# Optimization experiments

Measured on AMD Instinct MI355X. Metric: run time of the kernel, lower is better.

Reference implementation:

```python
import jax, jax.numpy as jnp
import numpy as np
from functools import partial

# Straight-through-estimator binarization: forward hard threshold,
# backward identity (matches BinaPs BinarizeTensorThresh autograd.Function).
@partial(jax.custom_vjp, nondiff_argnums=(1,))
def binarize(x, thresh):
    return (x >= thresh).astype(x.dtype)

def _bin_fwd(x, thresh):
    return binarize(x, thresh), None

def _bin_bwd(thresh, res, g):
    return (g,)

binarize.defvjp(_bin_fwd, _bin_bwd)

WEIGHT_THRESH = 0.5   # weightBClipValue passed to BinarizedLinearModule
ACT_THRESH = 1.0      # binary activation fires when pre-activation reaches 1


def setup_inputs() -> dict:
    key = jax.random.key(0)
    kx, kw = jax.random.split(key)
    B, D, H = 8192, 4096, 2048  # batch (transactions), features, hidden (patterns)
    x = (jax.random.uniform(kx, (B, D)) < 0.05).astype(jnp.float32)
    # Real-valued shared encoder weight, clipped to [-1, 1] by clipWeights();
    # init in [0, 1) so its 0.5-threshold binarization is non-trivial.
    W = jax.random.uniform(kw, (H, D), dtype=jnp.float32)
    b_enc = -jnp.ones((H,), jnp.float32)   # init_bias: vector of -1
    b0 = jnp.zeros((H,), jnp.float32)      # act0 bias (clipBias keeps <= 0)
    b3 = jnp.zeros((D,), jnp.float32)      # act3 bias (noBias forces 0)
    return {"x": x, "W": W, "b_enc": b_enc, "b0": b0, "b3": b3}


def reference(x, W, b_enc, b0, b3):
    # Binarize shared weight (encoder and transposed decoder use the same Wb)
    Wb = binarize(W, WEIGHT_THRESH)                      # [H, D] in {0,1}
    # Encoder: BinarizedLinear(D->H) with bias, then BinaryActivation
    h = binarize(x @ Wb.T + b_enc + b0, ACT_THRESH)      # [B, H] in {0,1}
    # Decoder: transposed shared weight, no bias, then final BinaryActivation
    out = binarize(h @ Wb + b3, ACT_THRESH)              # [B, D] in {0,1}
    return out
```

## Files before the change

kernel.cpp:

```cpp
#include <hip/hip_runtime.h>
#include <stdint.h>

#define BB 8192
#define DD 4096
#define HH 2048
#define DW (DD / 32)
#define HW (HH / 32)

__global__ void k_pack_x(const float* __restrict__ x,
                         uint32_t* __restrict__ xb) {
    int flat = blockIdx.x * blockDim.x + threadIdx.x;
    int b  = flat >> 7;
    int wd = flat & (DW - 1);
    const float4* p = (const float4*)(x + (size_t)b * DD + 32 * wd);
    uint32_t w = 0;
#pragma unroll
    for (int q = 0; q < 8; ++q) {
        float4 v = p[q];
        w |= (v.x >= 0.5f ? 1u : 0u) << (4 * q + 0);
        w |= (v.y >= 0.5f ? 1u : 0u) << (4 * q + 1);
        w |= (v.z >= 0.5f ? 1u : 0u) << (4 * q + 2);
        w |= (v.w >= 0.5f ? 1u : 0u) << (4 * q + 3);
    }
    xb[flat] = w;
}

__global__ void k_pack_wrow(const float* __restrict__ W,
                            uint32_t* __restrict__ WrowT4) {
    int flat = blockIdx.x * blockDim.x + threadIdx.x;
    int j = flat >> 7;
    int k = flat & (DW - 1);
    const float4* p = (const float4*)(W + (size_t)j * DD + 32 * k);
    uint32_t w = 0;
#pragma unroll
    for (int q = 0; q < 8; ++q) {
        float4 v = p[q];
        w |= (v.x >= 0.5f ? 1u : 0u) << (4 * q + 0);
        w |= (v.y >= 0.5f ? 1u : 0u) << (4 * q + 1);
        w |= (v.z >= 0.5f ? 1u : 0u) << (4 * q + 2);
        w |= (v.w >= 0.5f ? 1u : 0u) << (4 * q + 3);
    }
    WrowT4[((size_t)(k >> 2) * HH + j) * 4 + (k & 3)] = w;
}

__global__ void k_pack_wcol(const float* __restrict__ W,
                            uint32_t* __restrict__ WcolT) {
    int flat = blockIdx.x * blockDim.x + threadIdx.x;
    int kw = flat >> 12;
    int d  = flat & (DD - 1);
    uint32_t w = 0;
#pragma unroll
    for (int i = 0; i < 32; ++i) {
        float v = W[(size_t)(kw * 32 + i) * DD + d];
        w |= (v >= 0.5f ? 1u : 0u) << i;
    }
    WcolT[(size_t)kw * DD + d] = w;
}

__device__ __forceinline__ int calc_thresh(float bias) {
    float need = 1.0f - bias;
    if (!(need == need)) return 2000000000;
    if (need > 1.0e9f)  return 2000000000;
    if (need < -1.0e9f) return -2000000000;
    int t = (int)ceilf(need);
#pragma unroll
    for (int it = 0; it < 2; ++it)
        if ((float)(t - 1) + bias >= 1.0f) t--;
#pragma unroll
    for (int it = 0; it < 2; ++it)
        if ((float)t + bias < 1.0f) t++;
    return t;
}

__global__ void k_thresh(const float* __restrict__ b_enc,
                         const float* __restrict__ b0,
                         const float* __restrict__ b3,
                         int* __restrict__ t1, int* __restrict__ t2) {
    int tid = blockIdx.x * blockDim.x + threadIdx.x;
    if (tid < HH) {
        t1[tid] = calc_thresh(b_enc[tid] + b0[tid]);
    } else {
        int d = tid - HH;
        t2[d] = calc_thresh(b3[d]);
    }
}

__global__ void k_gemm1(const uint32_t* __restrict__ xb,
                        const uint4* __restrict__ WrowT4,
                        const int* __restrict__ t1,
                        uint32_t* __restrict__ hb) {
    int flat = blockIdx.x * blockDim.x + threadIdx.x;
    int b = flat >> 11;
    int j = flat & (HH - 1);
    const uint32_t* xr = xb + (size_t)b * DW;
    int t = t1[j];
    int c = 0;
    if (t > 0) {
        for (int k8 = 0; k8 < DW / 8; ++k8) {
            uint4 w0 = WrowT4[(size_t)(2 * k8) * HH + j];
            uint4 w1 = WrowT4[(size_t)(2 * k8 + 1) * HH + j];
            uint4 a0 = *(const uint4*)(xr + 8 * k8);
            uint4 a1 = *(const uint4*)(xr + 8 * k8 + 4);
            c += __popc(a0.x & w0.x) + __popc(a0.y & w0.y) +
                 __popc(a0.z & w0.z) + __popc(a0.w & w0.w) +
                 __popc(a1.x & w1.x) + __popc(a1.y & w1.y) +
                 __popc(a1.z & w1.z) + __popc(a1.w & w1.w);
            if (c >= t) break;
        }
    }
    unsigned long long m = __ballot(c >= t);
    if ((threadIdx.x & 63) == 0) {
        int jw = j >> 5;
        hb[(size_t)b * HW + jw]     = (uint32_t)m;
        hb[(size_t)b * HW + jw + 1] = (uint32_t)(m >> 32);
    }
}

__global__ void k_gemm2(const uint32_t* __restrict__ hb,
                        const uint32_t* __restrict__ WcolT,
                        const int* __restrict__ t2,
                        float* __restrict__ out) {
    int flat = blockIdx.x * blockDim.x + threadIdx.x;
    int b  = flat >> 10;
    int d0 = (flat & 1023) * 4;
    const uint32_t* hr = hb + (size_t)b * HW;
    int4 tt = *(const int4*)(t2 + d0);
    int c0 = 0, c1 = 0, c2 = 0, c3 = 0;
    for (int kw = 0; kw < HW; ++kw) {
        uint32_t h = hr[kw];
        uint4 w = *(const uint4*)(WcolT + (size_t)kw * DD + d0);
        c0 += __popc(h & w.x);
        c1 += __popc(h & w.y);
        c2 += __popc(h & w.z);
        c3 += __popc(h & w.w);
        if (c0 >= tt.x && c1 >= tt.y && c2 >= tt.z && c3 >= tt.w) break;
    }
    float4 r;
    r.x = (c0 >= tt.x) ? 1.0f : 0.0f;
    r.y = (c1 >= tt.y) ? 1.0f : 0.0f;
    r.z = (c2 >= tt.z) ? 1.0f : 0.0f;
    r.w = (c3 >= tt.w) ? 1.0f : 0.0f;
    *(float4*)(out + (size_t)b * DD + d0) = r;
}

extern "C" void kernel_launch(void* const* d_in, const int* in_sizes, int n_in,
                              void* d_out, int out_size, void* d_ws, size_t ws_size,
                              hipStream_t stream) {
    const float* x     = (const float*)d_in[0];
    const float* W     = (const float*)d_in[1];
    const float* b_enc = (const float*)d_in[2];
    const float* b0    = (const float*)d_in[3];
    const float* b3    = (const float*)d_in[4];
    float* out = (float*)d_out;

    char* ws = (char*)d_ws;
    uint32_t* WrowT4 = (uint32_t*)(ws);
    uint32_t* WcolT  = (uint32_t*)(ws + (1u << 20));
    uint32_t* xb     = (uint32_t*)(ws + (2u << 20));
    uint32_t* hb     = (uint32_t*)(ws + (6u << 20));
    int*      t1     = (int*)(ws + (8u << 20));
    int*      t2     = (int*)(ws + (8u << 20) + 8192);

    const int BLK = 256;

    k_pack_wrow<<<(HH * DW) / BLK, BLK, 0, stream>>>(W, WrowT4);
    k_pack_wcol<<<(HW * DD) / BLK, BLK, 0, stream>>>(W, WcolT);
    k_pack_x  <<<(BB * DW) / BLK, BLK, 0, stream>>>(x, xb);
    k_thresh  <<<(HH + DD) / BLK, BLK, 0, stream>>>(b_enc, b0, b3, t1, t2);
    k_gemm1   <<<(BB * HH) / BLK, BLK, 0, stream>>>(xb, (const uint4*)WrowT4, t1, hb);
    k_gemm2   <<<(BB * DD / 4) / BLK, BLK, 0, stream>>>(hb, WcolT, t2, out);
}
```

Before: 325.0 us.

## Fuse weight packing via LDS transpose and compute four batch rows per gemm1 thread

The two weight-packing kernels become one tiled kernel. It reads W once with coalesced float4 loads and builds the column-packed copy by transposing bits through shared memory, replacing the strided column reads. gemm1 now has each thread handle four batch rows for the same hidden unit, so every loaded packed-weight word is reused four times. The cost is an early exit that only fires when all four rows pass the threshold, plus higher register pressure from four accumulators.

Measured after the change: 304.5 us. 6.3% less time.

```diff
diff --git a/kernel.cpp b/kernel.cpp
--- a/kernel.cpp
+++ b/kernel.cpp
@@ -25,12 +25,20 @@
     xb[flat] = w;
 }
 
-__global__ void k_pack_wrow(const float* __restrict__ W,
-                            uint32_t* __restrict__ WrowT4) {
-    int flat = blockIdx.x * blockDim.x + threadIdx.x;
-    int j = flat >> 7;
-    int k = flat & (DW - 1);
-    const float4* p = (const float4*)(W + (size_t)j * DD + 32 * k);
+__global__ void __launch_bounds__(256)
+k_pack_w(const float* __restrict__ W,
+         uint32_t* __restrict__ WrowT4,
+         uint32_t* __restrict__ WcolT) {
+    __shared__ uint32_t lds[32][8];
+    int tile = blockIdx.x;
+    int jt = tile >> 4;
+    int dt = tile & 15;
+    int j0 = jt * 32;
+    int d0 = dt * 256;
+
+    int r  = threadIdx.x >> 3;
+    int wi = threadIdx.x & 7;
+    const float4* p = (const float4*)(W + (size_t)(j0 + r) * DD + d0 + wi * 32);
     uint32_t w = 0;
 #pragma unroll
     for (int q = 0; q < 8; ++q) {
@@ -40,21 +48,20 @@
         w |= (v.z >= 0.5f ? 1u : 0u) << (4 * q + 2);
         w |= (v.w >= 0.5f ? 1u : 0u) << (4 * q + 3);
     }
-    WrowT4[((size_t)(k >> 2) * HH + j) * 4 + (k & 3)] = w;
-}
-
-__global__ void k_pack_wcol(const float* __restrict__ W,
-                            uint32_t* __restrict__ WcolT) {
-    int flat = blockIdx.x * blockDim.x + threadIdx.x;
-    int kw = flat >> 12;
-    int d  = flat & (DD - 1);
-    uint32_t w = 0;
+    int k = dt * 8 + wi;
+    WrowT4[((size_t)(k >> 2) * HH + (j0 + r)) * 4 + (k & 3)] = w;
+    lds[r][wi] = w;
+    __syncthreads();
+
+    int dl = threadIdx.x;
+    int wsel = dl >> 5;
+    int bsel = dl & 31;
+    uint32_t cw = 0;
 #pragma unroll
     for (int i = 0; i < 32; ++i) {
-        float v = W[(size_t)(kw * 32 + i) * DD + d];
-        w |= (v >= 0.5f ? 1u : 0u) << i;
-    }
-    WcolT[(size_t)kw * DD + d] = w;
+        cw |= ((lds[i][wsel] >> bsel) & 1u) << i;
+    }
+    WcolT[(size_t)jt * DD + d0 + dl] = cw;
 }
 
 __device__ __forceinline__ int calc_thresh(float bias) {
@@ -90,29 +97,64 @@
                         const int* __restrict__ t1,
                         uint32_t* __restrict__ hb) {
     int flat = blockIdx.x * blockDim.x + threadIdx.x;
-    int b = flat >> 11;
-    int j = flat & (HH - 1);
-    const uint32_t* xr = xb + (size_t)b * DW;
+    int bg = flat >> 11;
+    int j  = flat & (HH - 1);
+    int b0 = bg * 4;
+    const uint32_t* xr0 = xb + (size_t)(b0 + 0) * DW;
+    const uint32_t* xr1 = xb + (size_t)(b0 + 1) * DW;
+    const uint32_t* xr2 = xb + (size_t)(b0 + 2) * DW;
+    const uint32_t* xr3 = xb + (size_t)(b0 + 3) * DW;
     int t = t1[j];
-    int c = 0;
+    int c0 = 0, c1 = 0, c2 = 0, c3 = 0;
     if (t > 0) {
         for (int k8 = 0; k8 < DW / 8; ++k8) {
             uint4 w0 = WrowT4[(size_t)(2 * k8) * HH + j];
             uint4 w1 = WrowT4[(size_t)(2 * k8 + 1) * HH + j];
-            uint4 a0 = *(const uint4*)(xr + 8 * k8);
-            uint4 a1 = *(const uint4*)(xr + 8 * k8 + 4);
-            c += __popc(a0.x & w0.x) + __popc(a0.y & w0.y) +
-                 __popc(a0.z & w0.z) + __popc(a0.w & w0.w) +
-                 __popc(a1.x & w1.x) + __popc(a1.y & w1.y) +
-                 __popc(a1.z & w1.z) + __popc(a1.w & w1.w);
-            if (c >= t) break;
+            uint4 a0, a1;
+            a0 = *(const uint4*)(xr0 + 8 * k8); a1 = *(const uint4*)(xr0 + 8 * k8 + 4);
+            c0 += __popc(a0.x & w0.x) + __popc(a0.y & w0.y) +
+                  __popc(a0.z & w0.z) + __popc(a0.w & w0.w) +
+                  __popc(a1.x & w1.x) + __popc(a1.y & w1.y) +
+                  __popc(a1.z & w1.z) + __popc(a1.w & w1.w);
+            a0 = *(const uint4*)(xr1 + 8 * k8); a1 = *(const uint4*)(xr1 + 8 * k8 + 4);
+            c1 += __popc(a0.x & w0.x) + __popc(a0.y & w0.y) +
+                  __popc(a0.z & w0.z) + __popc(a0.w & w0.w) +
+                  __popc(a1.x & w1.x) + __popc(a1.y & w1.y) +
+                  __popc(a1.z & w1.z) + __popc(a1.w & w1.w);
+            a0 = *(const uint4*)(xr2 + 8 * k8); a1 = *(const uint4*)(xr2 + 8 * k8 + 4);
+            c2 += __popc(a0.x & w0.x) + __popc(a0.y & w0.y) +
+                  __popc(a0.z & w0.z) + __popc(a0.w & w0.w) +
+                  __popc(a1.x & w1.x) + __popc(a1.y & w1.y) +
+                  __popc(a1.z & w1.z) + __popc(a1.w & w1.w);
+            a0 = *(const uint4*)(xr3 + 8 * k8); a1 = *(const uint4*)(xr3 + 8 * k8 + 4);
+            c3 += __popc(a0.x & w0.x) + __popc(a0.y & w0.y) +
+                  __popc(a0.z & w0.z) + __popc(a0.w & w0.w) +
+                  __popc(a1.x & w1.x) + __popc(a1.y & w1.y) +
+                  __popc(a1.z & w1.z) + __popc(a1.w & w1.w);
+            if (c0 >= t && c1 >= t && c2 >= t && c3 >= t) break;
         }
     }
-    unsigned long long m = __ballot(c >= t);
-    if ((threadIdx.x & 63) == 0) {
-        int jw = j >> 5;
-        hb[(size_t)b * HW + jw]     = (uint32_t)m;
-        hb[(size_t)b * HW + jw + 1] = (uint32_t)(m >> 32);
+    int jw = (j >> 5) & ~1;
+    unsigned long long m;
+    m = __ballot(c0 >= t);
+    if ((threadIdx.x & 63) == 0) {
+        hb[(size_t)(b0 + 0) * HW + jw]     = (uint32_t)m;
+        hb[(size_t)(b0 + 0) * HW + jw + 1] = (uint32_t)(m >> 32);
+    }
+    m = __ballot(c1 >= t);
+    if ((threadIdx.x & 63) == 0) {
+        hb[(size_t)(b0 + 1) * HW + jw]     = (uint32_t)m;
+        hb[(size_t)(b0 + 1) * HW + jw + 1] = (uint32_t)(m >> 32);
+    }
+    m = __ballot(c2 >= t);
+    if ((threadIdx.x & 63) == 0) {
+        hb[(size_t)(b0 + 2) * HW + jw]     = (uint32_t)m;
+        hb[(size_t)(b0 + 2) * HW + jw + 1] = (uint32_t)(m >> 32);
+    }
+    m = __ballot(c3 >= t);
+    if ((threadIdx.x & 63) == 0) {
+        hb[(size_t)(b0 + 3) * HW + jw]     = (uint32_t)m;
+        hb[(size_t)(b0 + 3) * HW + jw + 1] = (uint32_t)(m >> 32);
     }
 }
 
@@ -163,10 +205,9 @@
 
     const int BLK = 256;
 
-    k_pack_wrow<<<(HH * DW) / BLK, BLK, 0, stream>>>(W, WrowT4);
-    k_pack_wcol<<<(HW * DD) / BLK, BLK, 0, stream>>>(W, WcolT);
-    k_pack_x  <<<(BB * DW) / BLK, BLK, 0, stream>>>(x, xb);
-    k_thresh  <<<(HH + DD) / BLK, BLK, 0, stream>>>(b_enc, b0, b3, t1, t2);
-    k_gemm1   <<<(BB * HH) / BLK, BLK, 0, stream>>>(xb, (const uint4*)WrowT4, t1, hb);
-    k_gemm2   <<<(BB * DD / 4) / BLK, BLK, 0, stream>>>(hb, WcolT, t2, out);
-}
+    k_pack_w <<<(HH / 32) * (DD / 256), BLK, 0, stream>>>(W, WrowT4, WcolT);
+    k_pack_x <<<(BB * DW) / BLK, BLK, 0, stream>>>(x, xb);
+    k_thresh <<<(HH + DD) / BLK, BLK, 0, stream>>>(b_enc, b0, b3, t1, t2);
+    k_gemm1  <<<((BB / 4) * HH) / BLK, BLK, 0, stream>>>(xb, (const uint4*)WrowT4, t1, hb);
+    k_gemm2  <<<(BB * DD / 4) / BLK, BLK, 0, stream>>>(hb, WcolT, t2, out);
+}
```
